# Kernel tuning notes

Measured on AMD Instinct MI355X. Metric: run time of the kernel, lower is better.

## Reference

```python
import jax, jax.numpy as jnp
import numpy as np

NUM_PHRASES = 24
TOPN = 32
N = NUM_PHRASES * TOPN  # 768 graph nodes (phrase-box candidates)
D = 1024                # visual_dim
NUM_PAIRS = 24          # connected phrase pairs -> E = NUM_PAIRS * TOPN^2 = 24576 edges
STEPS = 1               # cfg.MODEL.RELATION.VISUAL_GRAPH_PASSING_TIME


def _build_graph():
    """Deterministic sparse connectivity: edges between all boxes of connected phrase pairs,
    ordered row-major like np.where(conn_map >= 0) in the original."""
    rng = np.random.default_rng(0)
    pairs = set()
    while len(pairs) < NUM_PAIRS:
        p1, p2 = rng.integers(0, NUM_PHRASES, size=2)
        if p1 != p2:
            pairs.add((int(p1), int(p2)))
    pairs = sorted(pairs)
    sbj_list, obj_list = [], []
    for p1, p2 in pairs:
        s = np.arange(TOPN) + p1 * TOPN
        o = np.arange(TOPN) + p2 * TOPN
        ss, oo = np.meshgrid(s, o, indexing='ij')
        sbj_list.append(ss.ravel())
        obj_list.append(oo.ravel())
    sbj = np.concatenate(sbj_list)
    obj = np.concatenate(obj_list)
    order = np.lexsort((obj, sbj))  # np.where row-major order
    sbj, obj = sbj[order], obj[order]
    involved = np.zeros(N, dtype=bool)
    for p1, p2 in pairs:
        involved[p1 * TOPN:(p1 + 1) * TOPN] = True
        involved[p2 * TOPN:(p2 + 1) * TOPN] = True
    return sbj.astype(np.int32), obj.astype(np.int32), involved


def setup_inputs() -> dict:
    sbj, obj, involved = _build_graph()
    E = sbj.shape[0]
    key = jax.random.key(0)
    ks = jax.random.split(key, 8)
    def w(k, shape, fan_in):
        return jax.random.normal(k, shape, dtype=jnp.float32) / np.float32(np.sqrt(fan_in))
    zD = jnp.zeros((D,), jnp.float32)
    return {
        "visual_feat": jax.random.normal(ks[0], (N, D), jnp.float32),
        "rel_visual_feat": jax.random.normal(ks[1], (E, D), jnp.float32),
        "W_rel": w(ks[2], (3 * D, D), 3 * D), "b_rel": zD,
        "W_sbj": w(ks[3], (2 * D, D), 2 * D), "b_sbj": zD,
        "W_obj": w(ks[4], (2 * D, D), 2 * D), "b_obj": zD,
        "W_ctx": w(ks[5], (D, D), D), "b_ctx": zD,
        "sbj_ind": jnp.asarray(sbj),
        "obj_ind": jnp.asarray(obj),
        "involved_mask": jnp.asarray(involved),
    }


def _edge_softmax(logits, seg, num_segments):
    # masked softmax over the sparse connectivity, normalized per segment (row or column)
    m = jax.ops.segment_max(logits, seg, num_segments=num_segments)
    e = jnp.exp(logits - m[seg])
    s = jax.ops.segment_sum(e, seg, num_segments=num_segments)
    return e / s[seg]


def reference(visual_feat, rel_visual_feat, W_rel, b_rel, W_sbj, b_sbj,
              W_obj, b_obj, W_ctx, b_ctx, sbj_ind, obj_ind, involved_mask):
    n, d = visual_feat.shape
    scale = np.float32(1.0 / np.sqrt(d))
    # split concat-Linear weights so we never materialize [E, 3D]/[E, 2D] concats
    Wr_s, Wr_o, Wr_r = W_rel[:d], W_rel[d:2 * d], W_rel[2 * d:]
    Ws_v, Ws_r = W_sbj[:d], W_sbj[d:]
    Wo_v, Wo_r = W_obj[:d], W_obj[d:]
    vj = visual_feat
    for _ in range(STEPS):
        vs = vj[sbj_ind]          # [E, D] gather
        vo = vj[obj_ind]          # [E, D] gather
        rel = vs @ Wr_s + vo @ Wr_o + rel_visual_feat @ Wr_r + b_rel  # rel_update_embedding
        ts = vs @ Ws_v + rel @ Ws_r + b_sbj   # visual_joint_trans_sbj
        to = vo @ Wo_v + rel @ Wo_r + b_obj   # visual_joint_trans_obj
        logits = jnp.sum(ts * to, axis=1) * scale  # [E]
        w_sbj = _edge_softmax(logits, sbj_ind, n)  # softmax over dim=1 (per subject row)
        w_obj = _edge_softmax(logits, obj_ind, n)  # softmax over dim=0 (per object col)
        # ctx[i] = sum_j w_sbj[i,j] * vj[j] + sum_j w_obj[j,i] * vj[j]  (sparse scatter-add)
        ctx = jax.ops.segment_sum(w_sbj[:, None] * vo, sbj_ind, num_segments=n) \
            + jax.ops.segment_sum(w_obj[:, None] * vs, obj_ind, num_segments=n)
        upd = vj + ctx @ W_ctx + b_ctx  # residual + visual_ctx_embedding, involved nodes only
        vj = jnp.where(involved_mask[:, None], upd, vj)
    return (rel_visual_feat, vj)
```

## Files before the change

### kernel.cpp

```cpp
#include <hip/hip_runtime.h>
#include <hip/hip_bf16.h>
#include <math.h>
#include <type_traits>

typedef __bf16 v8bf __attribute__((ext_vector_type(8)));
typedef __bf16 v4bf __attribute__((ext_vector_type(4)));
typedef float  v4f  __attribute__((ext_vector_type(4)));

__device__ __forceinline__ float wave_reduce_sum(float v) {
#pragma unroll
    for (int m = 1; m < 64; m <<= 1) v += __shfl_xor(v, m, 64);
    return v;
}

__device__ __forceinline__ unsigned fenc(float x) {
    unsigned u = __float_as_uint(x);
    return (u & 0x80000000u) ? ~u : (u | 0x80000000u);
}
__device__ __forceinline__ float fdec(unsigned k) {
    return (k & 0x80000000u) ? __uint_as_float(k ^ 0x80000000u) : __uint_as_float(~k);
}

__device__ __forceinline__ void gload16(const void* g, void* l) {
    __builtin_amdgcn_global_load_lds((const __attribute__((address_space(1))) void*)g,
                                     (__attribute__((address_space(3))) void*)l, 16, 0, 0);
}


__global__ __launch_bounds__(256) void cvt_f32_bf16(const float* __restrict__ in,
                                                    __bf16* __restrict__ out, long long n) {
    long long i = ((long long)blockIdx.x * 256 + threadIdx.x) * 4;
    if (i >= n) return;
    v4f v = *(const v4f*)(in + i);
    v4bf o;
    o[0] = (__bf16)v[0]; o[1] = (__bf16)v[1]; o[2] = (__bf16)v[2]; o[3] = (__bf16)v[3];
    *(v4bf*)(out + i) = o;
}

__global__ __launch_bounds__(256) void copy_cvt(const float* __restrict__ in,
                                                float* __restrict__ outCopy,
                                                __bf16* __restrict__ outB, long long n) {
    long long i = ((long long)blockIdx.x * 256 + threadIdx.x) * 4;
    if (i >= n) return;
    v4f v = *(const v4f*)(in + i);
    *(v4f*)(outCopy + i) = v;
    v4bf o;
    o[0] = (__bf16)v[0]; o[1] = (__bf16)v[1]; o[2] = (__bf16)v[2]; o[3] = (__bf16)v[3];
    *(v4bf*)(outB + i) = o;
}

__global__ __launch_bounds__(256) void cvt_t_bf16(const float* __restrict__ in,
                                                  __bf16* __restrict__ out, int R, int C) {
    __shared__ float tile[32][33];
    int cb = blockIdx.x * 32, rb = blockIdx.y * 32;
    int tx = threadIdx.x & 31, ty = threadIdx.x >> 5;
#pragma unroll
    for (int i = 0; i < 32; i += 8)
        tile[ty + i][tx] = in[(size_t)(rb + ty + i) * C + cb + tx];
    __syncthreads();
#pragma unroll
    for (int i = 0; i < 32; i += 8)
        out[(size_t)(cb + ty + i) * R + rb + tx] = (__bf16)tile[tx][ty + i];
}

__global__ __launch_bounds__(256) void cvt_t4_bf16(
    const float* __restrict__ in0, __bf16* __restrict__ out0,
    const float* __restrict__ in1, __bf16* __restrict__ out1,
    const float* __restrict__ in2, __bf16* __restrict__ out2,
    const float* __restrict__ in3, __bf16* __restrict__ out3, int Dd) {
    __shared__ float tile[32][33];
    const float* in = (blockIdx.z == 0) ? in0 : (blockIdx.z == 1) ? in1 : (blockIdx.z == 2) ? in2 : in3;
    __bf16* out = (blockIdx.z == 0) ? out0 : (blockIdx.z == 1) ? out1 : (blockIdx.z == 2) ? out2 : out3;
    int cb = blockIdx.x * 32, rb = blockIdx.y * 32;
    int tx = threadIdx.x & 31, ty = threadIdx.x >> 5;
#pragma unroll
    for (int i = 0; i < 32; i += 8)
        tile[ty + i][tx] = in[(size_t)(rb + ty + i) * Dd + cb + tx];
    __syncthreads();
#pragma unroll
    for (int i = 0; i < 32; i += 8)
        out[(size_t)(cb + ty + i) * Dd + rb + tx] = (__bf16)tile[tx][ty + i];
}

template <int MODE, bool BIG>
__global__ __launch_bounds__(256, 4) void gemm_gl(
    const __bf16* __restrict__ Ap, int ldA,
    const __bf16* __restrict__ Btp, int ldB,
    int M, int N, int K,
    long zA, long zB, long zOut,
    const float* __restrict__ addMat, int ldAdd,
    float* __restrict__ outF,
    __bf16* __restrict__ outB, int ldOut,
    __bf16* __restrict__ outB2,
    const __bf16* __restrict__ rbDot,
    float* __restrict__ qOut,
    const float* __restrict__ addRow,
    const int* __restrict__ maskRow,
    const int* __restrict__ sbjI,
    const int* __restrict__ objI) {
    constexpr int BM = BIG ? 128 : 64;
    constexpr int BN = BIG ? 128 : 64;
    constexpr int WM = BM / 2, WN = BN / 2;
    constexpr int FI = WM / 16, FJ = WN / 16;
    constexpr int NLA = (BM * 64) / 2048;
    constexpr int NLB = (BN * 64) / 2048;

    __shared__ alignas(16) __bf16 As[BM * 64];
    __shared__ alignas(16) __bf16 Bs[BN * 64];

    Ap  += zA * (long)blockIdx.z;
    Btp += zB * (long)blockIdx.z;
    outF += zOut * (long)blockIdx.z;

    const int m0 = blockIdx.x * BM, n0 = blockIdx.y * BN;
    const int t = threadIdx.x, lane = t & 63, wid = t >> 6;
    const int wm = wid >> 1, wn = wid & 1;
    const int rA = t >> 3;
    const int cSw = (t & 7) ^ (rA & 7);

    v4f acc[FI][FJ] = {};

    const int l15 = lane & 15;
    const int xorMask = (l15 & 7) << 4;

    for (int kt = 0; kt < K; kt += 64) {
#pragma unroll
        for (int i = 0; i < NLA; ++i)
            gload16(Ap + (size_t)(m0 + i * 32 + rA) * ldA + kt + cSw * 8,
                    (char*)As + i * 4096 + wid * 1024);
#pragma unroll
        for (int i = 0; i < NLB; ++i)
            gload16(Btp + (size_t)(n0 + i * 32 + rA) * ldB + kt + cSw * 8,
                    (char*)Bs + i * 4096 + wid * 1024);
        __syncthreads();
#pragma unroll
        for (int ks = 0; ks < 2; ++ks) {
            const int kb = (ks * 64 + ((lane >> 4) << 4)) ^ xorMask;
            v8bf af[FI], bfr[FJ];
#pragma unroll
            for (int f = 0; f < FI; ++f)
                af[f] = *(const v8bf*)((const char*)As + (wm * WM + f * 16 + l15) * 128 + kb);
#pragma unroll
            for (int f = 0; f < FJ; ++f)
                bfr[f] = *(const v8bf*)((const char*)Bs + (wn * WN + f * 16 + l15) * 128 + kb);
#pragma unroll
            for (int i = 0; i < FI; ++i)
#pragma unroll
                for (int j = 0; j < FJ; ++j)
                    acc[i][j] = __builtin_amdgcn_mfma_f32_16x16x32_bf16(af[i], bfr[j], acc[i][j], 0, 0, 0);
        }
        __syncthreads();
    }

    const int cc = lane & 15, r4 = (lane >> 4) << 2;
    if constexpr (MODE == 3) {
#pragma unroll
        for (int i = 0; i < FI; ++i)
#pragma unroll
            for (int r = 0; r < 4; ++r) {
                const int gm = m0 + wm * WM + i * 16 + r4 + r;
                const int s = sbjI[gm], o = objI[gm];
                const float* Ps = addMat + (size_t)s * ldAdd;
                const float* Qo = outF + (size_t)o * ldAdd;
                float p = 0.f;
#pragma unroll
                for (int j = 0; j < FJ; ++j) {
                    const int gn = n0 + wn * WN + j * 16 + cc;
                    float rv = (float)rbDot[(size_t)gm * N + gn];
                    p += rv * (acc[i][j][r] + Ps[gn] + Qo[gn] + addRow[gn]);
                }
                p += __shfl_xor(p, 1, 64);
                p += __shfl_xor(p, 2, 64);
                p += __shfl_xor(p, 4, 64);
                p += __shfl_xor(p, 8, 64);
                if (cc == 0) atomicAdd(qOut + gm, p);
            }
    } else if constexpr (MODE == 6) {
        const int mb = m0 >> 10, nb = n0 >> 10;
        const int blk = (mb == 0) ? (nb ? 3 : 1) : (nb ? 2 : 0);
        const __bf16* addB = (blk == 0) ? rbDot : (blk == 3 ? outB2 : nullptr);
        const size_t DDe = (size_t)ldOut * ldOut;
        __bf16* dst = outB + (size_t)blk * DDe;
#pragma unroll
        for (int i = 0; i < FI; ++i)
#pragma unroll
            for (int j = 0; j < FJ; ++j)
#pragma unroll
                for (int r = 0; r < 4; ++r) {
                    const int gml = (m0 + wm * WM + i * 16 + r4 + r) & 1023;
                    const int gnl = (n0 + wn * WN + j * 16 + cc) & 1023;
                    float v = acc[i][j][r];
                    if (addB) v += (float)addB[(size_t)gml * ldOut + gnl];
                    dst[(size_t)gml * ldOut + gnl] = (__bf16)v;
                }
    } else {
#pragma unroll
        for (int i = 0; i < FI; ++i)
#pragma unroll
            for (int j = 0; j < FJ; ++j)
#pragma unroll
                for (int r = 0; r < 4; ++r) {
                    const int gm = m0 + wm * WM + i * 16 + r4 + r;
                    const int gn = n0 + wn * WN + j * 16 + cc;
                    float v = acc[i][j][r];
                    if constexpr (MODE == 0) {
                        if (addMat) v += addMat[(size_t)gm * ldAdd + gn];
                        outB[(size_t)gm * ldOut + gn] = (__bf16)v;
                    } else if constexpr (MODE == 2) {
                        outF[(size_t)gm * ldOut + gn] = v;
                    } else {
                        float u = addMat[(size_t)gm * ldAdd + gn];
                        if (maskRow[gm]) u += v + addRow[gn];
                        outF[(size_t)gm * ldOut + gn] = u;
                    }
                }
    }
}


__global__ __launch_bounds__(256) void beta_kernel(
    const float* __restrict__ b_rel, const float* __restrict__ b_sbj, const float* __restrict__ b_obj,
    const float* __restrict__ Wsr, const float* __restrict__ Wor,
    float* __restrict__ bs, float* __restrict__ bo, int D, int rowsPerChunk) {
    const int col = blockIdx.x * 256 + threadIdx.x;
    if (col >= D) return;
    const int r0 = blockIdx.y * rowsPerChunk;
    const float* W = (blockIdx.z == 0) ? Wsr : Wor;
    float acc = 0.f;
    if (blockIdx.y == 0) acc = (blockIdx.z == 0) ? b_sbj[col] : b_obj[col];
    const int rEnd = min(r0 + rowsPerChunk, D);
    for (int r = r0; r < rEnd; ++r)
        acc += b_rel[r] * W[(size_t)r * D + col];
    float* out = (blockIdx.z == 0) ? bs : bo;
    atomicAdd(out + col, acc);
}

__global__ __launch_bounds__(256) void pbeta_kernel(const float* __restrict__ bs,
                                                    const float* __restrict__ bo,
                                                    const __bf16* __restrict__ KoKs,
                                                    float* __restrict__ pb, int D) {
    int d = blockIdx.x * 4 + (threadIdx.x >> 6);
    int lane = threadIdx.x & 63;
    float a = 0.f;
    for (int j = lane; j < D; j += 64)
        a += bs[j] * (float)KoKs[(size_t)d * 2048 + j] + bo[j] * (float)KoKs[(size_t)d * 2048 + 1024 + j];
    a = wave_reduce_sum(a);
    if (lane == 0) pb[d] = a;
}

__global__ __launch_bounds__(256) void node_kernel(
    const __bf16* __restrict__ ACBD,
    const float* __restrict__ bs, const float* __restrict__ bo,
    float* __restrict__ nodeS, float* __restrict__ nodeO, int D) {
    int n = blockIdx.x * 4 + (threadIdx.x >> 6);
    int lane = threadIdx.x & 63;
    int d0 = lane * 16;
    const __bf16* row = ACBD + (size_t)n * 4 * D;
    const __bf16* pa = row + d0;
    const __bf16* pc = row + D + d0;
    const __bf16* pB = row + 2 * D + d0;
    const __bf16* pd = row + 3 * D + d0;
    float s1 = 0.f, s2 = 0.f;
#pragma unroll
    for (int u = 0; u < 16; ++u) {
        float a = (float)pa[u], c = (float)pc[u], b = (float)pB[u], dd = (float)pd[u];
        float vs_ = bs[d0 + u], vo_ = bo[d0 + u];
        s1 += a * c + a * vo_ + vs_ * c;
        s2 += b * dd + b * vo_ + vs_ * dd;
    }
    s1 = wave_reduce_sum(s1);
    s2 = wave_reduce_sum(s2);
    if (lane == 0) { nodeS[n] = s1; nodeO[n] = s2; }
}

__global__ __launch_bounds__(256) void edge_lmax_kernel(
    const float* __restrict__ q,
    const float* __restrict__ nodeS, const float* __restrict__ nodeO,
    const float* __restrict__ G_AD, const float* __restrict__ G_BC,
    const int* __restrict__ sbj, const int* __restrict__ obj,
    float* __restrict__ logits, unsigned* __restrict__ mS, unsigned* __restrict__ mO,
    int E, int Nn, float scale) {
    int e = blockIdx.x * 256 + threadIdx.x;
    if (e >= E) return;
    int s = sbj[e], o = obj[e];
    float l = (q[e] + nodeS[s] + nodeO[o] +
               G_AD[(size_t)s * Nn + o] + G_BC[(size_t)o * Nn + s]) * scale;
    logits[e] = l;
    unsigned k = fenc(l);
    atomicMax(mS + s, k);
    atomicMax(mO + o, k);
}

__global__ __launch_bounds__(256) void expsum_kernel(const float* __restrict__ logits,
                                                     const int* __restrict__ sbj,
                                                     const int* __restrict__ obj,
                                                     const unsigned* __restrict__ mS,
                                                     const unsigned* __restrict__ mO,
                                                     float* __restrict__ es, float* __restrict__ eo,
                                                     float* __restrict__ sumS, float* __restrict__ sumO,
                                                     int E) {
    int e = blockIdx.x * 256 + threadIdx.x;
    if (e >= E) return;
    float l = logits[e];
    int s = sbj[e], o = obj[e];
    float a = expf(l - fdec(mS[s]));
    es[e] = a;
    atomicAdd(sumS + s, a);
    float b = expf(l - fdec(mO[o]));
    eo[e] = b;
    atomicAdd(sumO + o, b);
}

__global__ __launch_bounds__(256) void scatter_kernel(const float* __restrict__ es,
                                                      const float* __restrict__ eo,
                                                      const float* __restrict__ sumS,
                                                      const float* __restrict__ sumO,
                                                      const int* __restrict__ sbj,
                                                      const int* __restrict__ obj,
                                                      float* __restrict__ S, int* __restrict__ inv,
                                                      int E, int Nn) {
    int e = blockIdx.x * 256 + threadIdx.x;
    if (e >= E) return;
    int s = sbj[e], o = obj[e];
    atomicAdd(S + (size_t)s * Nn + o, es[e] / sumS[s]);
    atomicAdd(S + (size_t)o * Nn + s, eo[e] / sumO[o]);
    inv[s] = 1;
    inv[o] = 1;
}


extern "C" void kernel_launch(void* const* d_in, const int* in_sizes, int n_in,
                              void* d_out, int out_size, void* d_ws, size_t ws_size,
                              hipStream_t stream) {
    const float* V     = (const float*)d_in[0];
    const float* relv  = (const float*)d_in[1];
    const float* W_rel = (const float*)d_in[2];
    const float* b_rel = (const float*)d_in[3];
    const float* W_sbj = (const float*)d_in[4];
    const float* b_sbj = (const float*)d_in[5];
    const float* W_obj = (const float*)d_in[6];
    const float* b_obj = (const float*)d_in[7];
    const float* W_ctx = (const float*)d_in[8];
    const float* b_ctx = (const float*)d_in[9];
    const int* sbj = (const int*)d_in[10];
    const int* obj = (const int*)d_in[11];

    const int D  = in_sizes[3];
    const int E  = in_sizes[10];
    const int Nn = in_sizes[12];
    const size_t DD = (size_t)D * D;

    const float* Ws_v = W_sbj;
    const float* Ws_r = W_sbj + DD;
    const float* Wo_v = W_obj;
    const float* Wo_r = W_obj + DD;

    char* ws = (char*)d_ws;
    size_t off = 0;
    auto alloc = [&](size_t bytes) -> void* {
        void* p = (void*)(ws + off);
        off += (bytes + 255) & ~(size_t)255;
        return p;
    };

    __bf16* relv_b = (__bf16*)alloc((size_t)E * D * 2);
    __bf16* Vb     = (__bf16*)alloc((size_t)Nn * D * 2);
    __bf16* VbT    = (__bf16*)alloc((size_t)D * Nn * 2);
    __bf16* ZT_b   = (__bf16*)alloc(DD * 2);
    __bf16* KoKs   = (__bf16*)alloc((size_t)D * 2 * D * 2);
    __bf16* ACBD   = (__bf16*)alloc((size_t)Nn * 4 * D * 2);
    __bf16* Ws_vT  = (__bf16*)alloc(DD * 2);
    __bf16* Wo_vT  = (__bf16*)alloc(DD * 2);
    size_t r1 = off;
    __bf16* Wr_all = (__bf16*)(ws + r1);
    float*  G_AD   = (float*)(ws + r1);
    float*  G_BC   = G_AD + (size_t)Nn * Nn;
    {
        size_t a = 3 * DD * 2, b = 2 * (size_t)Nn * Nn * 4;
        off += ((a > b ? a : b) + 255) & ~(size_t)255;
    }
    size_t r2 = off;
    __bf16* WoWs_T = (__bf16*)(ws + r2);
    __bf16* W_ctxT = (__bf16*)(ws + r2);
    off += 2 * DD * 2;
    size_t r3 = off;
    __bf16* MT_all = (__bf16*)(ws + r3);
    float*  Pm     = (float*)(ws + r3);
    float*  Qm     = Pm + (size_t)Nn * D;
    {
        size_t a = 4 * DD * 2, b = 2 * (size_t)Nn * D * 4;
        off += ((a > b ? a : b) + 255) & ~(size_t)255;
    }
    float* pb     = (float*)alloc((size_t)D * 4);
    float* nodeS  = (float*)alloc((size_t)Nn * 4);
    float* nodeO  = (float*)alloc((size_t)Nn * 4);
    float* logits = (float*)alloc((size_t)E * 4);
    float* es     = (float*)alloc((size_t)E * 4);
    float* eo     = (float*)alloc((size_t)E * 4);
    size_t zbeg = off;
    float* S      = (float*)alloc((size_t)Nn * Nn * 4);
    float* q      = (float*)alloc((size_t)E * 4);
    float* bs     = (float*)alloc((size_t)D * 4);
    float* bo     = (float*)alloc((size_t)D * 4);
    unsigned* mS  = (unsigned*)alloc((size_t)Nn * 4);
    unsigned* mO  = (unsigned*)alloc((size_t)Nn * 4);
    float* sumS   = (float*)alloc((size_t)Nn * 4);
    float* sumO   = (float*)alloc((size_t)Nn * 4);
    int* inv      = (int*)alloc((size_t)Nn * 4);
    size_t zend = off;
    __bf16* Sb    = (__bf16*)alloc((size_t)Nn * Nn * 2);
    __bf16* ctx_b = (__bf16*)alloc((size_t)Nn * D * 2);
    (void)ws_size; (void)n_in; (void)out_size;

    float* outVj = (float*)d_out + (size_t)E * D;

    hipMemsetAsync(ws + zbeg, 0, zend - zbeg, stream);

    auto cvt = [&](const float* in, __bf16* out, size_t n) {
        int blocks = (int)((n / 4 + 255) / 256);
        cvt_f32_bf16<<<dim3(blocks), dim3(256), 0, stream>>>(in, out, (long long)n);
    };
    auto cvtT = [&](const float* in, __bf16* out, int R, int C) {
        cvt_t_bf16<<<dim3(C / 32, R / 32), dim3(256), 0, stream>>>(in, out, R, C);
    };
    {
        long long n = (long long)E * D;
        copy_cvt<<<dim3((int)(n / 4 / 256)), dim3(256), 0, stream>>>(relv, (float*)d_out, relv_b, n);
    }
    cvt(W_rel, Wr_all, 3 * DD);
    cvt(V, Vb, (size_t)Nn * D);
    cvt_t4_bf16<<<dim3(D / 32, D / 32, 4), dim3(256), 0, stream>>>(
        Wo_r, WoWs_T, Ws_r, WoWs_T + DD, Ws_v, Ws_vT, Wo_v, Wo_vT, D);
    cvtT(V, VbT, Nn, D);

    beta_kernel<<<dim3((D + 255) / 256, 32, 2), dim3(256), 0, stream>>>(
        b_rel, b_sbj, b_obj, Ws_r, Wo_r, bs, bo, D, (D + 31) / 32);

    auto G = [&](auto modeTag, auto bigTag, const __bf16* A, int ldA, const __bf16* Bt, int ldB,
                 int M, int N2, int K, int nz, long zA, long zB, long zOut,
                 const float* addMat, int ldAdd, float* outF, __bf16* outB, int ldOut,
                 __bf16* outB2, const __bf16* rbD, float* qO, const float* addRow, const int* mask,
                 const int* sbjI = nullptr, const int* objI = nullptr) {
        constexpr int BT = decltype(bigTag)::value ? 128 : 64;
        gemm_gl<decltype(modeTag)::value, decltype(bigTag)::value>
            <<<dim3(M / BT, N2 / BT, nz), dim3(256), 0, stream>>>(
                A, ldA, Bt, ldB, M, N2, K, zA, zB, zOut, addMat, ldAdd, outF, outB, ldOut,
                outB2, rbD, qO, addRow, mask, sbjI, objI);
    };
    using M0 = std::integral_constant<int, 0>;
    using M2 = std::integral_constant<int, 2>;
    using M3 = std::integral_constant<int, 3>;
    using M4 = std::integral_constant<int, 4>;
    using M6 = std::integral_constant<int, 6>;
    using SMALL = std::integral_constant<bool, false>;
    using LARGE = std::integral_constant<bool, true>;

    G(M6{}, LARGE{}, WoWs_T, D, Wr_all, D, 2 * D, 2 * D, D, 1, 0, 0, 0,
      nullptr, 0, nullptr, MT_all, D, Wo_vT, Ws_vT, nullptr, nullptr, nullptr);
    G(M0{}, LARGE{}, Wr_all + 2 * DD, D, WoWs_T, D, D, 2 * D, D, 1, 0, 0, 0,
      nullptr, 0, nullptr, KoKs, 2 * D, nullptr, nullptr, nullptr, nullptr, nullptr);
    cvtT(W_ctx, W_ctxT, D, D);
    G(M0{}, SMALL{}, KoKs + 0, 2 * D, KoKs + D, 2 * D, D, D, D, 1, 0, 0, 0,
      nullptr, 0, nullptr, ZT_b, D, nullptr, nullptr, nullptr, nullptr, nullptr);
    pbeta_kernel<<<dim3(D / 4), dim3(256), 0, stream>>>(bs, bo, KoKs, pb, D);

    G(M0{}, SMALL{}, Vb, D, MT_all, D, Nn, 4 * D, D, 1, 0, 0, 0,
      nullptr, 0, nullptr, ACBD, 4 * D, nullptr, nullptr, nullptr, nullptr, nullptr);

    G(M2{}, SMALL{}, ACBD + 0 * D, 4 * D, ACBD + 3 * D, 4 * D, Nn, Nn, D, 2,
      2 * (long)D, -2 * (long)D, (long)Nn * Nn,
      nullptr, 0, G_AD, nullptr, Nn, nullptr, nullptr, nullptr, nullptr, nullptr);
    G(M2{}, SMALL{}, ACBD + 0 * D, 4 * D, KoKs, 2 * D, Nn, D, 2 * D, 2,
      2 * (long)D, 0, (long)Nn * D,
      nullptr, 0, Pm, nullptr, D, nullptr, nullptr, nullptr, nullptr, nullptr);

    node_kernel<<<dim3(Nn / 4), dim3(256), 0, stream>>>(ACBD, bs, bo, nodeS, nodeO, D);

    G(M3{}, LARGE{}, relv_b, D, ZT_b, D, E, D, D, 1, 0, 0, 0,
      Pm, D, Qm, nullptr, 0, nullptr, relv_b, q, pb, nullptr, sbj, obj);

    edge_lmax_kernel<<<dim3(E / 256), dim3(256), 0, stream>>>(
        q, nodeS, nodeO, G_AD, G_BC, sbj, obj, logits, mS, mO, E, Nn, 1.0f / sqrtf((float)D));
    expsum_kernel<<<dim3(E / 256), dim3(256), 0, stream>>>(logits, sbj, obj, mS, mO, es, eo, sumS, sumO, E);
    scatter_kernel<<<dim3(E / 256), dim3(256), 0, stream>>>(es, eo, sumS, sumO, sbj, obj, S, inv, E, Nn);

    cvt(S, Sb, (size_t)Nn * Nn);
    G(M0{}, SMALL{}, Sb, Nn, VbT, Nn, Nn, D, Nn, 1, 0, 0, 0,
      nullptr, 0, nullptr, ctx_b, D, nullptr, nullptr, nullptr, nullptr, nullptr);
    G(M4{}, SMALL{}, ctx_b, D, W_ctxT, D, Nn, D, D, 1, 0, 0, 0,
      V, D, outVj, nullptr, D, nullptr, nullptr, nullptr, b_ctx, inv);
}
```

Baseline: 374.0 us.

## Replace edge-dot GEMM with dedicated 8-wave double-buffered 256x128 kernel

Swaps the MODE 3 path of the generic GEMM (E x D x D with fused per-edge dot epilogue) for a specialised kernel. The new kernel uses 512 threads, a 256x128 tile, double-buffered LDS filled by direct global-to-LDS loads, and raises wave priority around the MFMA bursts. The aim is to overlap the next tile's loads with compute and get more reuse per block on the largest GEMM. It uses more LDS per block, which can lower occupancy, and the extra syncthreads per phase may add stalls.

```diff
diff --git a/kernel.cpp b/kernel.cpp
--- a/kernel.cpp
+++ b/kernel.cpp
@@ -80,6 +80,114 @@
 #pragma unroll
     for (int i = 0; i < 32; i += 8)
         out[(size_t)(cb + ty + i) * Dd + rb + tx] = (__bf16)tile[tx][ty + i];
+}
+
+__global__ __launch_bounds__(512) void gemm8_dot(
+    const __bf16* __restrict__ Ap,
+    const __bf16* __restrict__ Btp,
+    int M, int N, int K,
+    const float* __restrict__ Pm,
+    const float* __restrict__ Qm,
+    const float* __restrict__ pb,
+    const __bf16* __restrict__ rbDot,
+    float* __restrict__ qOut,
+    const int* __restrict__ sbjI,
+    const int* __restrict__ objI) {
+    constexpr int BM = 256, BN = 128, BK = 64;
+    __shared__ alignas(16) __bf16 lds[2 * (BM + BN) * BK];
+    __bf16* const As0 = lds;
+    __bf16* const Bs0 = lds + BM * BK;
+    __bf16* const As1 = lds + (BM + BN) * BK;
+    __bf16* const Bs1 = As1 + BM * BK;
+
+    const int m0 = blockIdx.x * BM, n0 = blockIdx.y * BN;
+    const int t = threadIdx.x, lane = t & 63, wid = t >> 6;
+    const int wm = wid >> 1, wn = wid & 1;
+    const int l15 = lane & 15;
+    const int xorMask = (l15 & 7) << 4;
+    const int rA = t >> 3;
+    const int cSw = (t & 7) ^ (rA & 7);
+
+    v4f acc[4][4] = {};
+    const int nt = K / BK;
+
+    auto STAGE = [&](__bf16* dA, __bf16* dB, int kt) {
+#pragma unroll
+        for (int i = 0; i < 4; ++i)
+            gload16(Ap + (size_t)(m0 + i * 64 + rA) * K + kt + cSw * 8,
+                    (char*)dA + i * 8192 + t * 16);
+#pragma unroll
+        for (int i = 0; i < 2; ++i)
+            gload16(Btp + (size_t)(n0 + i * 64 + rA) * K + kt + cSw * 8,
+                    (char*)dB + i * 8192 + t * 16);
+    };
+
+    STAGE(As0, Bs0, 0);
+    asm volatile("s_waitcnt vmcnt(0)");
+    __builtin_amdgcn_sched_barrier(0);
+    __syncthreads();
+
+    for (int tt = 0; tt < nt; ++tt) {
+        const int cur = tt & 1;
+        const __bf16* curA = cur ? As1 : As0;
+        const __bf16* curB = cur ? Bs1 : Bs0;
+        if (tt + 1 < nt) STAGE(cur ? As0 : As1, cur ? Bs0 : Bs1, (tt + 1) * BK);
+
+#pragma unroll
+        for (int ph = 0; ph < 4; ++ph) {
+            const int fiH = ph >> 1, fjH = ph & 1;
+            v8bf af[2][2], bfv[2][2];
+#pragma unroll
+            for (int fs = 0; fs < 2; ++fs)
+#pragma unroll
+                for (int ks = 0; ks < 2; ++ks) {
+                    const int kb = (ks * 64 + ((lane >> 4) << 4)) ^ xorMask;
+                    af[fs][ks] = *(const v8bf*)((const char*)curA +
+                                  (wm * 64 + (fiH * 2 + fs) * 16 + l15) * 128 + kb);
+                    bfv[fs][ks] = *(const v8bf*)((const char*)curB +
+                                  (wn * 64 + (fjH * 2 + fs) * 16 + l15) * 128 + kb);
+                }
+            __syncthreads();
+            asm volatile("s_waitcnt lgkmcnt(0)");
+            __builtin_amdgcn_sched_barrier(0);
+            __builtin_amdgcn_s_setprio(1);
+#pragma unroll
+            for (int ks = 0; ks < 2; ++ks)
+#pragma unroll
+                for (int i = 0; i < 2; ++i)
+#pragma unroll
+                    for (int j = 0; j < 2; ++j)
+                        acc[fiH * 2 + i][fjH * 2 + j] = __builtin_amdgcn_mfma_f32_16x16x32_bf16(
+                            af[i][ks], bfv[j][ks], acc[fiH * 2 + i][fjH * 2 + j], 0, 0, 0);
+            __builtin_amdgcn_s_setprio(0);
+        }
+        asm volatile("s_waitcnt vmcnt(0)");
+        __builtin_amdgcn_sched_barrier(0);
+        __syncthreads();
+    }
+
+    const int cc = lane & 15, r4 = (lane >> 4) << 2;
+#pragma unroll
+    for (int i = 0; i < 4; ++i)
+#pragma unroll
+        for (int r = 0; r < 4; ++r) {
+            const int gm = m0 + wm * 64 + i * 16 + r4 + r;
+            const int s = sbjI[gm], o = objI[gm];
+            const float* Ps = Pm + (size_t)s * N;
+            const float* Qo = Qm + (size_t)o * N;
+            float p = 0.f;
+#pragma unroll
+            for (int j = 0; j < 4; ++j) {
+                const int gn = n0 + wn * 64 + j * 16 + cc;
+                float rv = (float)rbDot[(size_t)gm * N + gn];
+                p += rv * (acc[i][j][r] + Ps[gn] + Qo[gn] + pb[gn]);
+            }
+            p += __shfl_xor(p, 1, 64);
+            p += __shfl_xor(p, 2, 64);
+            p += __shfl_xor(p, 4, 64);
+            p += __shfl_xor(p, 8, 64);
+            if (cc == 0) atomicAdd(qOut + gm, p);
+        }
 }
 
 template <int MODE, bool BIG>
@@ -153,29 +261,7 @@
     }
 
     const int cc = lane & 15, r4 = (lane >> 4) << 2;
-    if constexpr (MODE == 3) {
-#pragma unroll
-        for (int i = 0; i < FI; ++i)
-#pragma unroll
-            for (int r = 0; r < 4; ++r) {
-                const int gm = m0 + wm * WM + i * 16 + r4 + r;
-                const int s = sbjI[gm], o = objI[gm];
-                const float* Ps = addMat + (size_t)s * ldAdd;
-                const float* Qo = outF + (size_t)o * ldAdd;
-                float p = 0.f;
-#pragma unroll
-                for (int j = 0; j < FJ; ++j) {
-                    const int gn = n0 + wn * WN + j * 16 + cc;
-                    float rv = (float)rbDot[(size_t)gm * N + gn];
-                    p += rv * (acc[i][j][r] + Ps[gn] + Qo[gn] + addRow[gn]);
-                }
-                p += __shfl_xor(p, 1, 64);
-                p += __shfl_xor(p, 2, 64);
-                p += __shfl_xor(p, 4, 64);
-                p += __shfl_xor(p, 8, 64);
-                if (cc == 0) atomicAdd(qOut + gm, p);
-            }
-    } else if constexpr (MODE == 6) {
+    if constexpr (MODE == 6) {
         const int mb = m0 >> 10, nb = n0 >> 10;
         const int blk = (mb == 0) ? (nb ? 3 : 1) : (nb ? 2 : 0);
         const __bf16* addB = (blk == 0) ? rbDot : (blk == 3 ? outB2 : nullptr);
@@ -449,7 +535,6 @@
     };
     using M0 = std::integral_constant<int, 0>;
     using M2 = std::integral_constant<int, 2>;
-    using M3 = std::integral_constant<int, 3>;
     using M4 = std::integral_constant<int, 4>;
     using M6 = std::integral_constant<int, 6>;
     using SMALL = std::integral_constant<bool, false>;
@@ -476,8 +561,8 @@
 
     node_kernel<<<dim3(Nn / 4), dim3(256), 0, stream>>>(ACBD, bs, bo, nodeS, nodeO, D);
 
-    G(M3{}, LARGE{}, relv_b, D, ZT_b, D, E, D, D, 1, 0, 0, 0,
-      Pm, D, Qm, nullptr, 0, nullptr, relv_b, q, pb, nullptr, sbj, obj);
+    gemm8_dot<<<dim3(E / 256, D / 128), dim3(512), 0, stream>>>(
+        relv_b, ZT_b, E, D, D, Pm, Qm, pb, relv_b, q, sbj, obj);
 
     edge_lmax_kernel<<<dim3(E / 256), dim3(256), 0, stream>>>(
         q, nodeS, nodeO, G_AD, G_BC, sbj, obj, logits, mS, mO, E, Nn, 1.0f / sqrtf((float)D));
```

After: 403.8 us. 8.0% more time.

## Merge conversion and independent GEMM launches into fewer multi-task kernels

Applied to the files above, without the earlier changes.

Folds the three flat f32→bf16 conversions into one megacvt kernel, the five transposing conversions into one z-indexed kernel, and the two weight-precompute GEMMs into a single MODE 5 launch. Independent GEMMs (ZT and ACBD, then G_AD/G_BC/Pm/Qm) are grouped into pair and quad 64-tile kernels selected by blockIdx.z. The goal is fewer kernel launches and more concurrent blocks on small GEMMs. In exchange it adds per-block branching and some early-exit blocks, and the specialised kernels duplicate the GEMM body.

```diff
diff --git a/kernel.cpp b/kernel.cpp
--- a/kernel.cpp
+++ b/kernel.cpp
@@ -37,16 +37,31 @@
     *(v4bf*)(out + i) = o;
 }
 
-__global__ __launch_bounds__(256) void copy_cvt(const float* __restrict__ in,
-                                                float* __restrict__ outCopy,
-                                                __bf16* __restrict__ outB, long long n) {
+__global__ __launch_bounds__(256) void megacvt(
+    const float* __restrict__ relv, float* __restrict__ outCopy, __bf16* __restrict__ relv_b,
+    long long nr,
+    const float* __restrict__ wrel, __bf16* __restrict__ wrel_b, long long nw,
+    const float* __restrict__ vsrc, __bf16* __restrict__ v_b, long long nv) {
     long long i = ((long long)blockIdx.x * 256 + threadIdx.x) * 4;
-    if (i >= n) return;
-    v4f v = *(const v4f*)(in + i);
-    *(v4f*)(outCopy + i) = v;
-    v4bf o;
-    o[0] = (__bf16)v[0]; o[1] = (__bf16)v[1]; o[2] = (__bf16)v[2]; o[3] = (__bf16)v[3];
-    *(v4bf*)(outB + i) = o;
+    if (i < nr) {
+        v4f v = *(const v4f*)(relv + i);
+        *(v4f*)(outCopy + i) = v;
+        v4bf o;
+        o[0] = (__bf16)v[0]; o[1] = (__bf16)v[1]; o[2] = (__bf16)v[2]; o[3] = (__bf16)v[3];
+        *(v4bf*)(relv_b + i) = o;
+    } else if (i < nr + nw) {
+        long long j = i - nr;
+        v4f v = *(const v4f*)(wrel + j);
+        v4bf o;
+        o[0] = (__bf16)v[0]; o[1] = (__bf16)v[1]; o[2] = (__bf16)v[2]; o[3] = (__bf16)v[3];
+        *(v4bf*)(wrel_b + j) = o;
+    } else if (i < nr + nw + nv) {
+        long long j = i - nr - nw;
+        v4f v = *(const v4f*)(vsrc + j);
+        v4bf o;
+        o[0] = (__bf16)v[0]; o[1] = (__bf16)v[1]; o[2] = (__bf16)v[2]; o[3] = (__bf16)v[3];
+        *(v4bf*)(v_b + j) = o;
+    }
 }
 
 __global__ __launch_bounds__(256) void cvt_t_bf16(const float* __restrict__ in,
@@ -63,23 +78,32 @@
         out[(size_t)(cb + ty + i) * R + rb + tx] = (__bf16)tile[tx][ty + i];
 }
 
-__global__ __launch_bounds__(256) void cvt_t4_bf16(
+__global__ __launch_bounds__(256) void cvt_t5_bf16(
     const float* __restrict__ in0, __bf16* __restrict__ out0,
     const float* __restrict__ in1, __bf16* __restrict__ out1,
     const float* __restrict__ in2, __bf16* __restrict__ out2,
-    const float* __restrict__ in3, __bf16* __restrict__ out3, int Dd) {
+    const float* __restrict__ in3, __bf16* __restrict__ out3,
+    const float* __restrict__ in4, __bf16* __restrict__ out4,
+    int Dd, int Nn) {
     __shared__ float tile[32][33];
-    const float* in = (blockIdx.z == 0) ? in0 : (blockIdx.z == 1) ? in1 : (blockIdx.z == 2) ? in2 : in3;
-    __bf16* out = (blockIdx.z == 0) ? out0 : (blockIdx.z == 1) ? out1 : (blockIdx.z == 2) ? out2 : out3;
+    const float* in; __bf16* out; int R, C;
+    switch (blockIdx.z) {
+        case 0: in = in0; out = out0; R = Dd; C = Dd; break;
+        case 1: in = in1; out = out1; R = Dd; C = Dd; break;
+        case 2: in = in2; out = out2; R = Dd; C = Dd; break;
+        case 3: in = in3; out = out3; R = Dd; C = Dd; break;
+        default: in = in4; out = out4; R = Nn; C = Dd; break;
+    }
     int cb = blockIdx.x * 32, rb = blockIdx.y * 32;
+    if (cb >= C || rb >= R) return;
     int tx = threadIdx.x & 31, ty = threadIdx.x >> 5;
 #pragma unroll
     for (int i = 0; i < 32; i += 8)
-        tile[ty + i][tx] = in[(size_t)(rb + ty + i) * Dd + cb + tx];
+        tile[ty + i][tx] = in[(size_t)(rb + ty + i) * C + cb + tx];
     __syncthreads();
 #pragma unroll
     for (int i = 0; i < 32; i += 8)
-        out[(size_t)(cb + ty + i) * Dd + rb + tx] = (__bf16)tile[tx][ty + i];
+        out[(size_t)(cb + ty + i) * R + rb + tx] = (__bf16)tile[tx][ty + i];
 }
 
 template <int MODE, bool BIG>
@@ -87,7 +111,6 @@
     const __bf16* __restrict__ Ap, int ldA,
     const __bf16* __restrict__ Btp, int ldB,
     int M, int N, int K,
-    long zA, long zB, long zOut,
     const float* __restrict__ addMat, int ldAdd,
     float* __restrict__ outF,
     __bf16* __restrict__ outB, int ldOut,
@@ -97,7 +120,8 @@
     const float* __restrict__ addRow,
     const int* __restrict__ maskRow,
     const int* __restrict__ sbjI,
-    const int* __restrict__ objI) {
+    const int* __restrict__ objI,
+    const __bf16* __restrict__ auxW) {
     constexpr int BM = BIG ? 128 : 64;
     constexpr int BN = BIG ? 128 : 64;
     constexpr int WM = BM / 2, WN = BN / 2;
@@ -108,11 +132,18 @@
     __shared__ alignas(16) __bf16 As[BM * 64];
     __shared__ alignas(16) __bf16 Bs[BN * 64];
 
-    Ap  += zA * (long)blockIdx.z;
-    Btp += zB * (long)blockIdx.z;
-    outF += zOut * (long)blockIdx.z;
-
-    const int m0 = blockIdx.x * BM, n0 = blockIdx.y * BN;
+    int m0 = blockIdx.x * BM, n0 = blockIdx.y * BN;
+    bool kRows = false;
+    if constexpr (MODE == 5) {
+        if (m0 >= 2048) {
+            kRows = true;
+            const __bf16* t = Ap;
+            Ap = Btp + (size_t)2 * K * K;
+            Btp = t;
+            m0 -= 2048;
+        }
+    }
+
     const int t = threadIdx.x, lane = t & 63, wid = t >> 6;
     const int wm = wid >> 1, wn = wid & 1;
     const int rA = t >> 3;
@@ -175,24 +206,37 @@
                 p += __shfl_xor(p, 8, 64);
                 if (cc == 0) atomicAdd(qOut + gm, p);
             }
-    } else if constexpr (MODE == 6) {
-        const int mb = m0 >> 10, nb = n0 >> 10;
-        const int blk = (mb == 0) ? (nb ? 3 : 1) : (nb ? 2 : 0);
-        const __bf16* addB = (blk == 0) ? rbDot : (blk == 3 ? outB2 : nullptr);
-        const size_t DDe = (size_t)ldOut * ldOut;
-        __bf16* dst = outB + (size_t)blk * DDe;
-#pragma unroll
-        for (int i = 0; i < FI; ++i)
-#pragma unroll
-            for (int j = 0; j < FJ; ++j)
-#pragma unroll
-                for (int r = 0; r < 4; ++r) {
-                    const int gml = (m0 + wm * WM + i * 16 + r4 + r) & 1023;
-                    const int gnl = (n0 + wn * WN + j * 16 + cc) & 1023;
-                    float v = acc[i][j][r];
-                    if (addB) v += (float)addB[(size_t)gml * ldOut + gnl];
-                    dst[(size_t)gml * ldOut + gnl] = (__bf16)v;
-                }
+    } else if constexpr (MODE == 5) {
+        if (kRows) {
+#pragma unroll
+            for (int i = 0; i < FI; ++i)
+#pragma unroll
+                for (int j = 0; j < FJ; ++j)
+#pragma unroll
+                    for (int r = 0; r < 4; ++r) {
+                        const int gm = m0 + wm * WM + i * 16 + r4 + r;
+                        const int gn = n0 + wn * WN + j * 16 + cc;
+                        outB2[(size_t)gm * 2048 + gn] = (__bf16)acc[i][j][r];
+                    }
+        } else {
+            const int mb = m0 >> 10, nb = n0 >> 10;
+            const int blk = (mb == 0) ? (nb ? 3 : 1) : (nb ? 2 : 0);
+            const __bf16* addB = (blk == 0) ? rbDot : (blk == 3 ? auxW : nullptr);
+            const size_t DDe = (size_t)ldOut * ldOut;
+            __bf16* dst = outB + (size_t)blk * DDe;
+#pragma unroll
+            for (int i = 0; i < FI; ++i)
+#pragma unroll
+                for (int j = 0; j < FJ; ++j)
+#pragma unroll
+                    for (int r = 0; r < 4; ++r) {
+                        const int gml = (m0 + wm * WM + i * 16 + r4 + r) & 1023;
+                        const int gnl = (n0 + wn * WN + j * 16 + cc) & 1023;
+                        float v = acc[i][j][r];
+                        if (addB) v += (float)addB[(size_t)gml * ldOut + gnl];
+                        dst[(size_t)gml * ldOut + gnl] = (__bf16)v;
+                    }
+        }
     } else {
 #pragma unroll
         for (int i = 0; i < FI; ++i)
@@ -206,8 +250,6 @@
                     if constexpr (MODE == 0) {
                         if (addMat) v += addMat[(size_t)gm * ldAdd + gn];
                         outB[(size_t)gm * ldOut + gn] = (__bf16)v;
-                    } else if constexpr (MODE == 2) {
-                        outF[(size_t)gm * ldOut + gn] = v;
                     } else {
                         float u = addMat[(size_t)gm * ldAdd + gn];
                         if (maskRow[gm]) u += v + addRow[gn];
@@ -215,6 +257,132 @@
                     }
                 }
     }
+}
+
+__global__ __launch_bounds__(256, 4) void gemm64_pair(
+    const __bf16* __restrict__ A0, int ldA0, const __bf16* __restrict__ B0, int ldB0,
+    int M0v, int N0v, __bf16* __restrict__ O0, int ldO0,
+    const __bf16* __restrict__ A1, int ldA1, const __bf16* __restrict__ B1, int ldB1,
+    int M1v, int N1v, __bf16* __restrict__ O1, int ldO1, int K) {
+    const __bf16* Ap; const __bf16* Btp; __bf16* Ob;
+    int ldA, ldB, Mv, Nv, ldO;
+    if (blockIdx.z == 0) { Ap = A0; Btp = B0; Ob = O0; ldA = ldA0; ldB = ldB0; Mv = M0v; Nv = N0v; ldO = ldO0; }
+    else                 { Ap = A1; Btp = B1; Ob = O1; ldA = ldA1; ldB = ldB1; Mv = M1v; Nv = N1v; ldO = ldO1; }
+    const int m0 = blockIdx.x * 64, n0 = blockIdx.y * 64;
+    if (m0 >= Mv || n0 >= Nv) return;
+
+    __shared__ alignas(16) __bf16 As[64 * 64];
+    __shared__ alignas(16) __bf16 Bs[64 * 64];
+    const int t = threadIdx.x, lane = t & 63, wid = t >> 6;
+    const int wm = wid >> 1, wn = wid & 1;
+    const int rA = t >> 3;
+    const int cSw = (t & 7) ^ (rA & 7);
+    const int l15 = lane & 15;
+    const int xorMask = (l15 & 7) << 4;
+    v4f acc[2][2] = {};
+
+    for (int kt = 0; kt < K; kt += 64) {
+#pragma unroll
+        for (int i = 0; i < 2; ++i)
+            gload16(Ap + (size_t)(m0 + i * 32 + rA) * ldA + kt + cSw * 8,
+                    (char*)As + i * 4096 + wid * 1024);
+#pragma unroll
+        for (int i = 0; i < 2; ++i)
+            gload16(Btp + (size_t)(n0 + i * 32 + rA) * ldB + kt + cSw * 8,
+                    (char*)Bs + i * 4096 + wid * 1024);
+        __syncthreads();
+#pragma unroll
+        for (int ks = 0; ks < 2; ++ks) {
+            const int kb = (ks * 64 + ((lane >> 4) << 4)) ^ xorMask;
+            v8bf af[2], bfr[2];
+#pragma unroll
+            for (int f = 0; f < 2; ++f) {
+                af[f]  = *(const v8bf*)((const char*)As + (wm * 32 + f * 16 + l15) * 128 + kb);
+                bfr[f] = *(const v8bf*)((const char*)Bs + (wn * 32 + f * 16 + l15) * 128 + kb);
+            }
+#pragma unroll
+            for (int i = 0; i < 2; ++i)
+#pragma unroll
+                for (int j = 0; j < 2; ++j)
+                    acc[i][j] = __builtin_amdgcn_mfma_f32_16x16x32_bf16(af[i], bfr[j], acc[i][j], 0, 0, 0);
+        }
+        __syncthreads();
+    }
+    const int cc = lane & 15, r4 = (lane >> 4) << 2;
+#pragma unroll
+    for (int i = 0; i < 2; ++i)
+#pragma unroll
+        for (int j = 0; j < 2; ++j)
+#pragma unroll
+            for (int r = 0; r < 4; ++r) {
+                const int gm = m0 + wm * 32 + i * 16 + r4 + r;
+                const int gn = n0 + wn * 32 + j * 16 + cc;
+                Ob[(size_t)gm * ldO + gn] = (__bf16)acc[i][j][r];
+            }
+}
+
+__global__ __launch_bounds__(256, 4) void gemm64_quad(
+    const __bf16* __restrict__ ACBD, const __bf16* __restrict__ KoKs,
+    float* __restrict__ G_AD, float* __restrict__ G_BC,
+    float* __restrict__ Pm, float* __restrict__ Qm, int Nn, int Dd) {
+    const int z = blockIdx.z;
+    const __bf16* Ap = ACBD + (size_t)(z & 1) * 2 * Dd;
+    const int ldA = 4 * Dd;
+    const __bf16* Btp; int ldB, Nv, K; float* Of; int ldO;
+    if (z == 0)      { Btp = ACBD + 3 * Dd; ldB = 4 * Dd; Nv = Nn; K = Dd;     Of = G_AD; ldO = Nn; }
+    else if (z == 1) { Btp = ACBD + 1 * Dd; ldB = 4 * Dd; Nv = Nn; K = Dd;     Of = G_BC; ldO = Nn; }
+    else             { Btp = KoKs;          ldB = 2 * Dd; Nv = Dd; K = 2 * Dd; Of = (z == 2) ? Pm : Qm; ldO = Dd; }
+    const int m0 = blockIdx.x * 64, n0 = blockIdx.y * 64;
+    if (n0 >= Nv) return;
+
+    __shared__ alignas(16) __bf16 As[64 * 64];
+    __shared__ alignas(16) __bf16 Bs[64 * 64];
+    const int t = threadIdx.x, lane = t & 63, wid = t >> 6;
+    const int wm = wid >> 1, wn = wid & 1;
+    const int rA = t >> 3;
+    const int cSw = (t & 7) ^ (rA & 7);
+    const int l15 = lane & 15;
+    const int xorMask = (l15 & 7) << 4;
+    v4f acc[2][2] = {};
+
+    for (int kt = 0; kt < K; kt += 64) {
+#pragma unroll
+        for (int i = 0; i < 2; ++i)
+            gload16(Ap + (size_t)(m0 + i * 32 + rA) * ldA + kt + cSw * 8,
+                    (char*)As + i * 4096 + wid * 1024);
+#pragma unroll
+        for (int i = 0; i < 2; ++i)
+            gload16(Btp + (size_t)(n0 + i * 32 + rA) * ldB + kt + cSw * 8,
+                    (char*)Bs + i * 4096 + wid * 1024);
+        __syncthreads();
+#pragma unroll
+        for (int ks = 0; ks < 2; ++ks) {
+            const int kb = (ks * 64 + ((lane >> 4) << 4)) ^ xorMask;
+            v8bf af[2], bfr[2];
+#pragma unroll
+            for (int f = 0; f < 2; ++f) {
+                af[f]  = *(const v8bf*)((const char*)As + (wm * 32 + f * 16 + l15) * 128 + kb);
+                bfr[f] = *(const v8bf*)((const char*)Bs + (wn * 32 + f * 16 + l15) * 128 + kb);
+            }
+#pragma unroll
+            for (int i = 0; i < 2; ++i)
+#pragma unroll
+                for (int j = 0; j < 2; ++j)
+                    acc[i][j] = __builtin_amdgcn_mfma_f32_16x16x32_bf16(af[i], bfr[j], acc[i][j], 0, 0, 0);
+        }
+        __syncthreads();
+    }
+    const int cc = lane & 15, r4 = (lane >> 4) << 2;
+#pragma unroll
+    for (int i = 0; i < 2; ++i)
+#pragma unroll
+        for (int j = 0; j < 2; ++j)
+#pragma unroll
+            for (int r = 0; r < 4; ++r) {
+                const int gm = m0 + wm * 32 + i * 16 + r4 + r;
+                const int gn = n0 + wn * 32 + j * 16 + cc;
+                Of[(size_t)gm * ldO + gn] = acc[i][j][r];
+            }
 }
 
 
@@ -416,77 +584,53 @@
 
     hipMemsetAsync(ws + zbeg, 0, zend - zbeg, stream);
 
-    auto cvt = [&](const float* in, __bf16* out, size_t n) {
-        int blocks = (int)((n / 4 + 255) / 256);
-        cvt_f32_bf16<<<dim3(blocks), dim3(256), 0, stream>>>(in, out, (long long)n);
-    };
-    auto cvtT = [&](const float* in, __bf16* out, int R, int C) {
-        cvt_t_bf16<<<dim3(C / 32, R / 32), dim3(256), 0, stream>>>(in, out, R, C);
-    };
     {
-        long long n = (long long)E * D;
-        copy_cvt<<<dim3((int)(n / 4 / 256)), dim3(256), 0, stream>>>(relv, (float*)d_out, relv_b, n);
-    }
-    cvt(W_rel, Wr_all, 3 * DD);
-    cvt(V, Vb, (size_t)Nn * D);
-    cvt_t4_bf16<<<dim3(D / 32, D / 32, 4), dim3(256), 0, stream>>>(
-        Wo_r, WoWs_T, Ws_r, WoWs_T + DD, Ws_v, Ws_vT, Wo_v, Wo_vT, D);
-    cvtT(V, VbT, Nn, D);
+        long long nr = (long long)E * D, nw = 3 * (long long)DD, nv = (long long)Nn * D;
+        long long total = nr + nw + nv;
+        int blocks = (int)((total / 4 + 255) / 256);
+        megacvt<<<dim3(blocks), dim3(256), 0, stream>>>(
+            relv, (float*)d_out, relv_b, nr, W_rel, Wr_all, nw, V, Vb, nv);
+    }
+    cvt_t5_bf16<<<dim3(D / 32, D / 32, 5), dim3(256), 0, stream>>>(
+        Wo_r, WoWs_T, Ws_r, WoWs_T + DD, Ws_v, Ws_vT, Wo_v, Wo_vT, V, VbT, D, Nn);
 
     beta_kernel<<<dim3((D + 255) / 256, 32, 2), dim3(256), 0, stream>>>(
         b_rel, b_sbj, b_obj, Ws_r, Wo_r, bs, bo, D, (D + 31) / 32);
 
-    auto G = [&](auto modeTag, auto bigTag, const __bf16* A, int ldA, const __bf16* Bt, int ldB,
-                 int M, int N2, int K, int nz, long zA, long zB, long zOut,
-                 const float* addMat, int ldAdd, float* outF, __bf16* outB, int ldOut,
-                 __bf16* outB2, const __bf16* rbD, float* qO, const float* addRow, const int* mask,
-                 const int* sbjI = nullptr, const int* objI = nullptr) {
-        constexpr int BT = decltype(bigTag)::value ? 128 : 64;
-        gemm_gl<decltype(modeTag)::value, decltype(bigTag)::value>
-            <<<dim3(M / BT, N2 / BT, nz), dim3(256), 0, stream>>>(
-                A, ldA, Bt, ldB, M, N2, K, zA, zB, zOut, addMat, ldAdd, outF, outB, ldOut,
-                outB2, rbD, qO, addRow, mask, sbjI, objI);
-    };
-    using M0 = std::integral_constant<int, 0>;
-    using M2 = std::integral_constant<int, 2>;
-    using M3 = std::integral_constant<int, 3>;
-    using M4 = std::integral_constant<int, 4>;
-    using M6 = std::integral_constant<int, 6>;
-    using SMALL = std::integral_constant<bool, false>;
-    using LARGE = std::integral_constant<bool, true>;
-
-    G(M6{}, LARGE{}, WoWs_T, D, Wr_all, D, 2 * D, 2 * D, D, 1, 0, 0, 0,
-      nullptr, 0, nullptr, MT_all, D, Wo_vT, Ws_vT, nullptr, nullptr, nullptr);
-    G(M0{}, LARGE{}, Wr_all + 2 * DD, D, WoWs_T, D, D, 2 * D, D, 1, 0, 0, 0,
-      nullptr, 0, nullptr, KoKs, 2 * D, nullptr, nullptr, nullptr, nullptr, nullptr);
-    cvtT(W_ctx, W_ctxT, D, D);
-    G(M0{}, SMALL{}, KoKs + 0, 2 * D, KoKs + D, 2 * D, D, D, D, 1, 0, 0, 0,
-      nullptr, 0, nullptr, ZT_b, D, nullptr, nullptr, nullptr, nullptr, nullptr);
+    gemm_gl<5, true><<<dim3(24, 16), dim3(256), 0, stream>>>(
+        WoWs_T, D, Wr_all, D, 3 * D, 2 * D, D, nullptr, 0, nullptr, MT_all, D,
+        KoKs, Ws_vT, nullptr, nullptr, nullptr, nullptr, nullptr, Wo_vT);
+
+    cvt_t_bf16<<<dim3(D / 32, D / 32), dim3(256), 0, stream>>>(W_ctx, W_ctxT, D, D);
+
+    gemm64_pair<<<dim3(16, 64, 2), dim3(256), 0, stream>>>(
+        KoKs + 0, 2 * D, KoKs + D, 2 * D, D, D, ZT_b, D,
+        Vb, D, MT_all, D, Nn, 4 * D, ACBD, 4 * D, D);
+
     pbeta_kernel<<<dim3(D / 4), dim3(256), 0, stream>>>(bs, bo, KoKs, pb, D);
 
-    G(M0{}, SMALL{}, Vb, D, MT_all, D, Nn, 4 * D, D, 1, 0, 0, 0,
-      nullptr, 0, nullptr, ACBD, 4 * D, nullptr, nullptr, nullptr, nullptr, nullptr);
-
-    G(M2{}, SMALL{}, ACBD + 0 * D, 4 * D, ACBD + 3 * D, 4 * D, Nn, Nn, D, 2,
-      2 * (long)D, -2 * (long)D, (long)Nn * Nn,
-      nullptr, 0, G_AD, nullptr, Nn, nullptr, nullptr, nullptr, nullptr, nullptr);
-    G(M2{}, SMALL{}, ACBD + 0 * D, 4 * D, KoKs, 2 * D, Nn, D, 2 * D, 2,
-      2 * (long)D, 0, (long)Nn * D,
-      nullptr, 0, Pm, nullptr, D, nullptr, nullptr, nullptr, nullptr, nullptr);
+    gemm64_quad<<<dim3(Nn / 64, 16, 4), dim3(256), 0, stream>>>(
+        ACBD, KoKs, G_AD, G_BC, Pm, Qm, Nn, D);
 
     node_kernel<<<dim3(Nn / 4), dim3(256), 0, stream>>>(ACBD, bs, bo, nodeS, nodeO, D);
 
-    G(M3{}, LARGE{}, relv_b, D, ZT_b, D, E, D, D, 1, 0, 0, 0,
-      Pm, D, Qm, nullptr, 0, nullptr, relv_b, q, pb, nullptr, sbj, obj);
+    gemm_gl<3, true><<<dim3(E / 128, D / 128), dim3(256), 0, stream>>>(
+        relv_b, D, ZT_b, D, E, D, D, Pm, D, Qm, nullptr, 0, nullptr,
+        relv_b, q, pb, nullptr, sbj, obj, nullptr);
 
     edge_lmax_kernel<<<dim3(E / 256), dim3(256), 0, stream>>>(
         q, nodeS, nodeO, G_AD, G_BC, sbj, obj, logits, mS, mO, E, Nn, 1.0f / sqrtf((float)D));
     expsum_kernel<<<dim3(E / 256), dim3(256), 0, stream>>>(logits, sbj, obj, mS, mO, es, eo, sumS, sumO, E);
     scatter_kernel<<<dim3(E / 256), dim3(256), 0, stream>>>(es, eo, sumS, sumO, sbj, obj, S, inv, E, Nn);
 
-    cvt(S, Sb, (size_t)Nn * Nn);
-    G(M0{}, SMALL{}, Sb, Nn, VbT, Nn, Nn, D, Nn, 1, 0, 0, 0,
-      nullptr, 0, nullptr, ctx_b, D, nullptr, nullptr, nullptr, nullptr, nullptr);
-    G(M4{}, SMALL{}, ctx_b, D, W_ctxT, D, Nn, D, D, 1, 0, 0, 0,
-      V, D, outVj, nullptr, D, nullptr, nullptr, nullptr, b_ctx, inv);
-}
+    {
+        size_t n = (size_t)Nn * Nn;
+        cvt_f32_bf16<<<dim3((int)((n / 4 + 255) / 256)), dim3(256), 0, stream>>>(S, Sb, (long long)n);
+    }
+    gemm_gl<0, false><<<dim3(Nn / 64, D / 64), dim3(256), 0, stream>>>(
+        Sb, Nn, VbT, Nn, Nn, D, Nn, nullptr, 0, nullptr, ctx_b, D,
+        nullptr, nullptr, nullptr, nullptr, nullptr, nullptr, nullptr, nullptr);
+    gemm_gl<4, false><<<dim3(Nn / 64, D / 64), dim3(256), 0, stream>>>(
+        ctx_b, D, W_ctxT, D, Nn, D, D, V, D, outVj, nullptr, D,
+        nullptr, nullptr, nullptr, b_ctx, inv, nullptr, nullptr, nullptr);
+}
```

After: 333.2 us. 1.12x faster.
